# Performance work log

Measured on AMD Instinct MI355X. Metric: run time of the kernel, lower is better.

## Reference

```python
import jax, jax.numpy as jnp
import numpy as np
import math

HEADS = 8
DIM_HEAD = 64
DIM = HEADS * DIM_HEAD  # 512; to_v is Identity so dim must equal heads*dim_head
SCALE = DIM_HEAD ** -0.5


def get_slopes(n):
    def pow2(n):
        start = 2 ** (-2 ** (-(math.log2(n) - 3)))
        return [start * start ** i for i in range(n)]
    if math.log2(n).is_integer():
        return pow2(n)
    c = 2 ** math.floor(math.log2(n))
    return pow2(c) + get_slopes(2 * c)[0::2][: n - c]

SLOPES = jnp.asarray(np.array(get_slopes(HEADS), dtype=np.float32))


def setup_inputs() -> dict:
    key = jax.random.key(0)
    k1, k2, k3, k4 = jax.random.split(key, 4)
    b, n = 4, 2048
    x = jax.random.normal(k1, (b, n, DIM), dtype=jnp.float32)
    # positions: e.g. observation timestamps (days); uniform floats scaled to [0, 365)
    positions = jax.random.uniform(k2, (b, n), dtype=jnp.float32) * 365.0
    Wq = jax.random.normal(k3, (DIM, DIM), dtype=jnp.float32) * (DIM ** -0.5)
    Wk = jax.random.normal(k4, (DIM, DIM), dtype=jnp.float32) * (DIM ** -0.5)
    return {"x": x, "positions": positions, "Wq": Wq, "Wk": Wk}


def reference(x, positions, Wq, Wk):
    b, n, _ = x.shape
    # q, k projections (no bias); v = x (Identity)
    q = (x @ Wq.T).reshape(b, n, HEADS, DIM_HEAD).transpose(0, 2, 1, 3)  # b h n d
    k = (x @ Wk.T).reshape(b, n, HEADS, DIM_HEAD).transpose(0, 2, 1, 3)
    v = x.reshape(b, n, HEADS, DIM_HEAD).transpose(0, 2, 1, 3)
    dots = jnp.einsum('bhid,bhjd->bhij', q, k) * SCALE  # b h n n
    # relative_positions[b,i,j] = -|positions[b,j] - positions[b,i]|
    rel = -jnp.abs(positions[:, None, :] - positions[:, :, None])  # b n n
    alibi = SLOPES[None, :, None, None] * rel[:, None, :, :]  # b h n n
    attn = jax.nn.softmax(dots + alibi, axis=-1)
    out = jnp.einsum('bhij,bhjd->bhid', attn, v)  # b h n d
    return out.transpose(0, 2, 1, 3).reshape(b, n, DIM)
```

## Files before the change

### kernel.cpp

```cpp
#include <hip/hip_runtime.h>
#include <hip/hip_bf16.h>

typedef __bf16 bf16x8 __attribute__((ext_vector_type(8)));
typedef float f32x4 __attribute__((ext_vector_type(4)));
typedef float f32x16 __attribute__((ext_vector_type(16)));

__device__ inline unsigned short f2bf(float f) {
    __hip_bfloat16 h = __float2bfloat16(f);
    return __builtin_bit_cast(unsigned short, h);
}
__device__ inline unsigned pk2bf(float a, float b) {
    return (unsigned)f2bf(a) | ((unsigned)f2bf(b) << 16);
}
__device__ inline float exp2_fast(float x) {
    float r;
    asm("v_exp_f32 %0, %1" : "=v"(r) : "v"(x));
    return r;
}

#define QSCALE 0.1803368801111244f

__global__ __launch_bounds__(256) void xpose_v(const float* __restrict__ x,
                                               unsigned short* __restrict__ Vt) {
    const int tid = threadIdx.x;
    const int lane = tid & 63, w = tid >> 6;
    const int b = blockIdx.z, h = blockIdx.y;
    const int n = blockIdx.x * 256 + w * 64 + lane;
    const int np = (n & ~15) | (n & 3) | ((n & 4) << 1) | ((n & 8) >> 1);
    const size_t xrow = ((size_t)b * 2048 + n) * 512 + h * 64;
    const size_t vbase = ((size_t)(b * 8 + h) * 64) * 2048 + np;
#pragma unroll
    for (int d0 = 0; d0 < 64; d0 += 4) {
        float4 v = *reinterpret_cast<const float4*>(&x[xrow + d0]);
        Vt[vbase + (size_t)(d0 + 0) * 2048] = f2bf(v.x);
        Vt[vbase + (size_t)(d0 + 1) * 2048] = f2bf(v.y);
        Vt[vbase + (size_t)(d0 + 2) * 2048] = f2bf(v.z);
        Vt[vbase + (size_t)(d0 + 3) * 2048] = f2bf(v.w);
    }
}

__global__ __launch_bounds__(256) void gemm_qk(const float* __restrict__ x,
                                               const float* __restrict__ Wq,
                                               const float* __restrict__ Wk,
                                               unsigned short* __restrict__ Qb,
                                               unsigned short* __restrict__ Kb) {
    __shared__ __align__(16) unsigned short sA[128 * 40];
    __shared__ __align__(16) unsigned short sB[128 * 40];
    const int tid  = threadIdx.x;
    const int lane = tid & 63;
    const int wave = tid >> 6;
    const int wr = wave >> 1, wc = wave & 1;
    const int bm = blockIdx.x * 128;
    const int by = blockIdx.y;
    const float* __restrict__ Bsrc = (by < 4) ? Wq : Wk;
    unsigned short* __restrict__ C = (by < 4) ? Qb : Kb;
    const int bn = (by & 3) * 128;
    const float scale = (by < 4) ? QSCALE : 1.0f;
    const int tr = tid >> 1, th = (tid & 1) * 16;
    const int rl = lane & 15;
    const int kq = (lane >> 4) * 8;

    f32x4 acc[4][4];
#pragma unroll
    for (int m = 0; m < 4; ++m)
#pragma unroll
        for (int n = 0; n < 4; ++n) acc[m][n] = (f32x4){0.f, 0.f, 0.f, 0.f};

    for (int k0 = 0; k0 < 512; k0 += 32) {
        const float* ap = &x[(size_t)(bm + tr) * 512 + k0 + th];
        const float* bp = &Bsrc[(size_t)(bn + tr) * 512 + k0 + th];
        float4 a0 = *reinterpret_cast<const float4*>(ap);
        float4 a1 = *reinterpret_cast<const float4*>(ap + 4);
        float4 a2 = *reinterpret_cast<const float4*>(ap + 8);
        float4 a3 = *reinterpret_cast<const float4*>(ap + 12);
        float4 b0 = *reinterpret_cast<const float4*>(bp);
        float4 b1 = *reinterpret_cast<const float4*>(bp + 4);
        float4 b2 = *reinterpret_cast<const float4*>(bp + 8);
        float4 b3 = *reinterpret_cast<const float4*>(bp + 12);
        uint4 pa0 = {pk2bf(a0.x, a0.y), pk2bf(a0.z, a0.w), pk2bf(a1.x, a1.y), pk2bf(a1.z, a1.w)};
        uint4 pa1 = {pk2bf(a2.x, a2.y), pk2bf(a2.z, a2.w), pk2bf(a3.x, a3.y), pk2bf(a3.z, a3.w)};
        uint4 pb0 = {pk2bf(b0.x, b0.y), pk2bf(b0.z, b0.w), pk2bf(b1.x, b1.y), pk2bf(b1.z, b1.w)};
        uint4 pb1 = {pk2bf(b2.x, b2.y), pk2bf(b2.z, b2.w), pk2bf(b3.x, b3.y), pk2bf(b3.z, b3.w)};
        __syncthreads();
        *reinterpret_cast<uint4*>(&sA[tr * 40 + th])     = pa0;
        *reinterpret_cast<uint4*>(&sA[tr * 40 + th + 8]) = pa1;
        *reinterpret_cast<uint4*>(&sB[tr * 40 + th])     = pb0;
        *reinterpret_cast<uint4*>(&sB[tr * 40 + th + 8]) = pb1;
        __syncthreads();

        bf16x8 af[4], bfv[4];
#pragma unroll
        for (int m = 0; m < 4; ++m)
            af[m] = __builtin_bit_cast(bf16x8,
                *reinterpret_cast<const uint4*>(&sA[(wr * 64 + m * 16 + rl) * 40 + kq]));
#pragma unroll
        for (int n = 0; n < 4; ++n)
            bfv[n] = __builtin_bit_cast(bf16x8,
                *reinterpret_cast<const uint4*>(&sB[(wc * 64 + n * 16 + rl) * 40 + kq]));
#pragma unroll
        for (int m = 0; m < 4; ++m)
#pragma unroll
            for (int n = 0; n < 4; ++n)
                acc[m][n] = __builtin_amdgcn_mfma_f32_16x16x32_bf16(af[m], bfv[n], acc[m][n], 0, 0, 0);
    }

    const int rq = (lane >> 4) * 4;
#pragma unroll
    for (int m = 0; m < 4; ++m) {
        int r = bm + wr * 64 + m * 16 + rq;
#pragma unroll
        for (int n = 0; n < 4; ++n) {
            int c = bn + wc * 64 + n * 16 + rl;
#pragma unroll
            for (int reg = 0; reg < 4; ++reg)
                C[(size_t)(r + reg) * 512 + c] = f2bf(acc[m][n][reg] * scale);
        }
    }
}

__global__ __launch_bounds__(512, 4) void attn_fwd(const unsigned short* __restrict__ Q,
                                                   const unsigned short* __restrict__ Kb,
                                                   const unsigned short* __restrict__ Vt,
                                                   const float* __restrict__ pos,
                                                   float* __restrict__ Out) {
    __shared__ __align__(16) unsigned char smem[34304];
    char* k0b = (char*)smem;
    char* v0b = (char*)smem + 8192;
    char* k1b = (char*)smem + 16384;
    char* v1b = (char*)smem + 24576;
    float* p0b = (float*)(smem + 32768);
    float* p1b = (float*)(smem + 33024);
    float* sMl = (float*)(smem + 33280);

    const int tid  = threadIdx.x;
    const int lane = tid & 63;
    const int w    = tid >> 6;
    const int l31  = lane & 31;
    const int hi   = lane >> 5;
    const int qh   = w & 3;
    const int jp   = w >> 2;
    const int flat = blockIdx.x;
    const int xcd  = flat & 7;
    const int idx  = flat >> 3;
    const int bh   = xcd * 4 + (idx >> 4);
    const int qt   = idx & 15;
    const int b = bh >> 3, h = bh & 7;
    const int q0 = qt * 128 + qh * 32;
    const size_t rowbase = (size_t)b * 2048;
    const int hc = h * 64;
    const float slopeL = ldexpf(1.4426950408889634f, -(h + 1));

    bf16x8 qf0, qf1, qf2, qf3;
    {
        const unsigned short* qp = &Q[(rowbase + q0 + l31) * 512 + hc + hi * 8];
        qf0 = __builtin_bit_cast(bf16x8, *reinterpret_cast<const uint4*>(qp));
        qf1 = __builtin_bit_cast(bf16x8, *reinterpret_cast<const uint4*>(qp + 16));
        qf2 = __builtin_bit_cast(bf16x8, *reinterpret_cast<const uint4*>(qp + 32));
        qf3 = __builtin_bit_cast(bf16x8, *reinterpret_cast<const uint4*>(qp + 48));
    }
    const float ui = slopeL * pos[rowbase + q0 + l31];
    const bf16x8 ones = __builtin_bit_cast(bf16x8,
        (uint4){0x3F803F80u, 0x3F803F80u, 0x3F803F80u, 0x3F803F80u});

    f32x16 o0, o1, lacc;
#pragma unroll
    for (int r = 0; r < 16; ++r) { o0[r] = 0.f; o1[r] = 0.f; lacc[r] = 0.f; }

    const int sr  = tid >> 3;
    const int sce = (tid & 7) * 8;
    const int wbyte = sr * 128 + (((tid & 7) * 16) ^ ((sr & 7) << 4));
    const int kswz = (l31 & 7) << 4;

    uint4 ck, cv;
    float cpj = 0.f;

    auto stage = [&](int j0v) {
        ck = *reinterpret_cast<const uint4*>(&Kb[(rowbase + j0v + sr) * 512 + hc + sce]);
        cv = *reinterpret_cast<const uint4*>(&Vt[((size_t)bh * 64 + sr) * 2048 + j0v + sce]);
        if (tid < 64) cpj = pos[rowbase + j0v + tid];
    };
    auto writeb = [&](char* KB, char* VB, float* PB) {
        *reinterpret_cast<uint4*>(KB + wbyte) = ck;
        *reinterpret_cast<uint4*>(VB + wbyte) = cv;
        if (tid < 64) PB[tid] = slopeL * cpj;
    };
    auto compute = [&](const char* KB, const char* VB, const float* PB) {
        const char* kr = KB + (32 * jp + l31) * 128;
        f32x16 s;
#pragma unroll
        for (int r = 0; r < 16; ++r) s[r] = 0.f;
        __builtin_amdgcn_s_setprio(1);
#pragma unroll
        for (int ks = 0; ks < 4; ++ks) {
            bf16x8 kf = __builtin_bit_cast(bf16x8,
                *reinterpret_cast<const uint4*>(kr + ((ks * 32 + hi * 16) ^ kswz)));
            bf16x8 qq = (ks == 0) ? qf0 : (ks == 1) ? qf1 : (ks == 2) ? qf2 : qf3;
            s = __builtin_amdgcn_mfma_f32_32x32x16_bf16(kf, qq, s, 0, 0, 0);
        }
        __builtin_amdgcn_s_setprio(0);

#pragma unroll
        for (int t = 0; t < 4; ++t) {
            f32x4 u = *reinterpret_cast<const f32x4*>(&PB[32 * jp + 8 * t + 4 * hi]);
#pragma unroll
            for (int r = 0; r < 4; ++r)
                s[4 * t + r] = exp2_fast(s[4 * t + r] - fabsf(u[r] - ui));
        }

        bf16x8 pf0 = __builtin_bit_cast(bf16x8, (uint4){
            pk2bf(s[0], s[1]),  pk2bf(s[2], s[3]),   pk2bf(s[4], s[5]),   pk2bf(s[6], s[7])});
        bf16x8 pf1 = __builtin_bit_cast(bf16x8, (uint4){
            pk2bf(s[8], s[9]),  pk2bf(s[10], s[11]), pk2bf(s[12], s[13]), pk2bf(s[14], s[15])});

        const char* vr0 = VB + l31 * 128;
        const char* vr1 = VB + (32 + l31) * 128;
        __builtin_amdgcn_s_setprio(1);
#pragma unroll
        for (int ks = 0; ks < 2; ++ks) {
            const int cb = (64 * jp + ks * 32 + hi * 16) ^ kswz;
            bf16x8 v0 = __builtin_bit_cast(bf16x8, *reinterpret_cast<const uint4*>(vr0 + cb));
            bf16x8 v1 = __builtin_bit_cast(bf16x8, *reinterpret_cast<const uint4*>(vr1 + cb));
            bf16x8 pf = ks ? pf1 : pf0;
            o0 = __builtin_amdgcn_mfma_f32_32x32x16_bf16(v0, pf, o0, 0, 0, 0);
            o1 = __builtin_amdgcn_mfma_f32_32x32x16_bf16(v1, pf, o1, 0, 0, 0);
            lacc = __builtin_amdgcn_mfma_f32_32x32x16_bf16(ones, pf, lacc, 0, 0, 0);
        }
        __builtin_amdgcn_s_setprio(0);
    };

    stage(0);
    writeb(k0b, v0b, p0b);
    stage(64);
    __syncthreads();

    for (int t = 0; t < 32; t += 2) {
        writeb(k1b, v1b, p1b);
        if (t + 2 < 32) stage((t + 2) * 64);
        compute(k0b, v0b, p0b);
        __syncthreads();
        if (t + 2 < 32) {
            writeb(k0b, v0b, p0b);
            if (t + 3 < 32) stage((t + 3) * 64);
        }
        compute(k1b, v1b, p1b);
        __syncthreads();
    }

    const float lt = lacc[0];
    float* sM = (float*)smem;
    const int key = (lane & 7) << 2;
    if (jp == 1) {
        float* dst = sM + qh * 2048 + lane * 32;
#pragma unroll
        for (int i = 0; i < 4; ++i) {
            f32x4 t0 = {o0[4 * i], o0[4 * i + 1], o0[4 * i + 2], o0[4 * i + 3]};
            f32x4 t1 = {o1[4 * i], o1[4 * i + 1], o1[4 * i + 2], o1[4 * i + 3]};
            *reinterpret_cast<f32x4*>(dst + ((4 * i) ^ key))      = t0;
            *reinterpret_cast<f32x4*>(dst + ((16 + 4 * i) ^ key)) = t1;
        }
        sMl[qh * 64 + lane] = lt;
    }
    __syncthreads();
    if (jp == 0) {
        const float* src = sM + qh * 2048 + lane * 32;
#pragma unroll
        for (int i = 0; i < 4; ++i) {
            f32x4 t0 = *reinterpret_cast<const f32x4*>(src + ((4 * i) ^ key));
            f32x4 t1 = *reinterpret_cast<const f32x4*>(src + ((16 + 4 * i) ^ key));
#pragma unroll
            for (int r = 0; r < 4; ++r) { o0[4 * i + r] += t0[r]; o1[4 * i + r] += t1[r]; }
        }
        const float linv = 1.0f / (lt + sMl[qh * 64 + lane]);
        float* orow = &Out[(rowbase + q0 + l31) * 512 + hc];
#pragma unroll
        for (int t = 0; t < 4; ++t) {
            f32x4 a, c;
#pragma unroll
            for (int r = 0; r < 4; ++r) {
                a[r] = o0[4 * t + r] * linv;
                c[r] = o1[4 * t + r] * linv;
            }
            *reinterpret_cast<f32x4*>(orow + 8 * t + 4 * hi)      = a;
            *reinterpret_cast<f32x4*>(orow + 32 + 8 * t + 4 * hi) = c;
        }
    }
}

extern "C" void kernel_launch(void* const* d_in, const int* in_sizes, int n_in,
                              void* d_out, int out_size, void* d_ws, size_t ws_size,
                              hipStream_t stream) {
    const float* x   = (const float*)d_in[0];
    const float* pos = (const float*)d_in[1];
    const float* Wq  = (const float*)d_in[2];
    const float* Wk  = (const float*)d_in[3];
    float* out = (float*)d_out;

    unsigned short* Qb  = (unsigned short*)d_ws;
    unsigned short* Kbf = Qb  + 4194304;
    unsigned short* Vtb = Kbf + 4194304;

    xpose_v<<<dim3(8, 8, 4), dim3(256), 0, stream>>>(x, Vtb);
    gemm_qk<<<dim3(64, 8), dim3(256), 0, stream>>>(x, Wq, Wk, Qb, Kbf);
    attn_fwd<<<dim3(512), dim3(512), 0, stream>>>(Qb, Kbf, Vtb, pos, out);
}
```

Before: 92.90 us.

## Fold V transpose into QK GEMM launch; preload scaled positions; sum row totals in VALU

Removes the separate V-transpose kernel by adding extra blockIdx.y slices to the QK projection launch, which saves one kernel launch and lets the transpose overlap the GEMM. In attention, all scaled key positions for the batch row are loaded into shared memory once up front instead of being staged each tile. The softmax denominator is now accumulated as a scalar sum of exponentials plus a cross-lane shuffle, replacing the extra MFMA against a ones matrix. The trade-off is more LDS per block (42KB), which may reduce occupancy, and a different rounding path for the denominator: the sum uses fp32 p rather than bf16-rounded p.

```diff
diff --git a/kernel.cpp b/kernel.cpp
--- a/kernel.cpp
+++ b/kernel.cpp
@@ -20,38 +20,41 @@
 
 #define QSCALE 0.1803368801111244f
 
-__global__ __launch_bounds__(256) void xpose_v(const float* __restrict__ x,
-                                               unsigned short* __restrict__ Vt) {
-    const int tid = threadIdx.x;
-    const int lane = tid & 63, w = tid >> 6;
-    const int b = blockIdx.z, h = blockIdx.y;
-    const int n = blockIdx.x * 256 + w * 64 + lane;
-    const int np = (n & ~15) | (n & 3) | ((n & 4) << 1) | ((n & 8) >> 1);
-    const size_t xrow = ((size_t)b * 2048 + n) * 512 + h * 64;
-    const size_t vbase = ((size_t)(b * 8 + h) * 64) * 2048 + np;
-#pragma unroll
-    for (int d0 = 0; d0 < 64; d0 += 4) {
-        float4 v = *reinterpret_cast<const float4*>(&x[xrow + d0]);
-        Vt[vbase + (size_t)(d0 + 0) * 2048] = f2bf(v.x);
-        Vt[vbase + (size_t)(d0 + 1) * 2048] = f2bf(v.y);
-        Vt[vbase + (size_t)(d0 + 2) * 2048] = f2bf(v.z);
-        Vt[vbase + (size_t)(d0 + 3) * 2048] = f2bf(v.w);
-    }
-}
-
 __global__ __launch_bounds__(256) void gemm_qk(const float* __restrict__ x,
                                                const float* __restrict__ Wq,
                                                const float* __restrict__ Wk,
                                                unsigned short* __restrict__ Qb,
-                                               unsigned short* __restrict__ Kb) {
+                                               unsigned short* __restrict__ Kb,
+                                               unsigned short* __restrict__ Vt) {
     __shared__ __align__(16) unsigned short sA[128 * 40];
     __shared__ __align__(16) unsigned short sB[128 * 40];
     const int tid  = threadIdx.x;
+    const int by = blockIdx.y;
+
+    if (by >= 8) {
+        const int q = by - 8;
+        const int nl = tid & 127, hh = tid >> 7;
+        const int h = q * 2 + hh;
+        const int g = blockIdx.x * 128 + nl;
+        const int b = g >> 11, n = g & 2047;
+        const int np = (n & ~15) | (n & 3) | ((n & 4) << 1) | ((n & 8) >> 1);
+        const size_t xrow = ((size_t)b * 2048 + n) * 512 + h * 64;
+        const size_t vbase = ((size_t)(b * 8 + h) * 64) * 2048 + np;
+#pragma unroll
+        for (int d0 = 0; d0 < 64; d0 += 4) {
+            float4 v = *reinterpret_cast<const float4*>(&x[xrow + d0]);
+            Vt[vbase + (size_t)(d0 + 0) * 2048] = f2bf(v.x);
+            Vt[vbase + (size_t)(d0 + 1) * 2048] = f2bf(v.y);
+            Vt[vbase + (size_t)(d0 + 2) * 2048] = f2bf(v.z);
+            Vt[vbase + (size_t)(d0 + 3) * 2048] = f2bf(v.w);
+        }
+        return;
+    }
+
     const int lane = tid & 63;
     const int wave = tid >> 6;
     const int wr = wave >> 1, wc = wave & 1;
     const int bm = blockIdx.x * 128;
-    const int by = blockIdx.y;
     const float* __restrict__ Bsrc = (by < 4) ? Wq : Wk;
     unsigned short* __restrict__ C = (by < 4) ? Qb : Kb;
     const int bn = (by & 3) * 128;
@@ -123,14 +126,13 @@
                                                    const unsigned short* __restrict__ Vt,
                                                    const float* __restrict__ pos,
                                                    float* __restrict__ Out) {
-    __shared__ __align__(16) unsigned char smem[34304];
+    __shared__ __align__(16) unsigned char smem[42240];
     char* k0b = (char*)smem;
     char* v0b = (char*)smem + 8192;
     char* k1b = (char*)smem + 16384;
     char* v1b = (char*)smem + 24576;
-    float* p0b = (float*)(smem + 32768);
-    float* p1b = (float*)(smem + 33024);
-    float* sMl = (float*)(smem + 33280);
+    float* sPosT = (float*)(smem + 32768);
+    float* sMl   = (float*)(smem + 40960);
 
     const int tid  = threadIdx.x;
     const int lane = tid & 63;
@@ -159,12 +161,17 @@
         qf3 = __builtin_bit_cast(bf16x8, *reinterpret_cast<const uint4*>(qp + 48));
     }
     const float ui = slopeL * pos[rowbase + q0 + l31];
-    const bf16x8 ones = __builtin_bit_cast(bf16x8,
-        (uint4){0x3F803F80u, 0x3F803F80u, 0x3F803F80u, 0x3F803F80u});
-
-    f32x16 o0, o1, lacc;
-#pragma unroll
-    for (int r = 0; r < 16; ++r) { o0[r] = 0.f; o1[r] = 0.f; lacc[r] = 0.f; }
+
+    {
+        float4 v = reinterpret_cast<const float4*>(pos + rowbase)[tid];
+        reinterpret_cast<f32x4*>(sPosT)[tid] =
+            (f32x4){v.x * slopeL, v.y * slopeL, v.z * slopeL, v.w * slopeL};
+    }
+
+    float lloc = 0.f;
+    f32x16 o0, o1;
+#pragma unroll
+    for (int r = 0; r < 16; ++r) { o0[r] = 0.f; o1[r] = 0.f; }
 
     const int sr  = tid >> 3;
     const int sce = (tid & 7) * 8;
@@ -172,19 +179,16 @@
     const int kswz = (l31 & 7) << 4;
 
     uint4 ck, cv;
-    float cpj = 0.f;
 
     auto stage = [&](int j0v) {
         ck = *reinterpret_cast<const uint4*>(&Kb[(rowbase + j0v + sr) * 512 + hc + sce]);
         cv = *reinterpret_cast<const uint4*>(&Vt[((size_t)bh * 64 + sr) * 2048 + j0v + sce]);
-        if (tid < 64) cpj = pos[rowbase + j0v + tid];
     };
-    auto writeb = [&](char* KB, char* VB, float* PB) {
+    auto writeb = [&](char* KB, char* VB) {
         *reinterpret_cast<uint4*>(KB + wbyte) = ck;
         *reinterpret_cast<uint4*>(VB + wbyte) = cv;
-        if (tid < 64) PB[tid] = slopeL * cpj;
     };
-    auto compute = [&](const char* KB, const char* VB, const float* PB) {
+    auto compute = [&](const char* KB, const char* VB, int j0) {
         const char* kr = KB + (32 * jp + l31) * 128;
         f32x16 s;
 #pragma unroll
@@ -199,13 +203,18 @@
         }
         __builtin_amdgcn_s_setprio(0);
 
+        float ls = 0.f;
 #pragma unroll
         for (int t = 0; t < 4; ++t) {
-            f32x4 u = *reinterpret_cast<const f32x4*>(&PB[32 * jp + 8 * t + 4 * hi]);
-#pragma unroll
-            for (int r = 0; r < 4; ++r)
-                s[4 * t + r] = exp2_fast(s[4 * t + r] - fabsf(u[r] - ui));
-        }
+            f32x4 u = *reinterpret_cast<const f32x4*>(&sPosT[j0 + 32 * jp + 8 * t + 4 * hi]);
+#pragma unroll
+            for (int r = 0; r < 4; ++r) {
+                float p = exp2_fast(s[4 * t + r] - fabsf(u[r] - ui));
+                s[4 * t + r] = p;
+                ls += p;
+            }
+        }
+        lloc += ls;
 
         bf16x8 pf0 = __builtin_bit_cast(bf16x8, (uint4){
             pk2bf(s[0], s[1]),  pk2bf(s[2], s[3]),   pk2bf(s[4], s[5]),   pk2bf(s[6], s[7])});
@@ -223,30 +232,29 @@
             bf16x8 pf = ks ? pf1 : pf0;
             o0 = __builtin_amdgcn_mfma_f32_32x32x16_bf16(v0, pf, o0, 0, 0, 0);
             o1 = __builtin_amdgcn_mfma_f32_32x32x16_bf16(v1, pf, o1, 0, 0, 0);
-            lacc = __builtin_amdgcn_mfma_f32_32x32x16_bf16(ones, pf, lacc, 0, 0, 0);
         }
         __builtin_amdgcn_s_setprio(0);
     };
 
     stage(0);
-    writeb(k0b, v0b, p0b);
+    writeb(k0b, v0b);
     stage(64);
     __syncthreads();
 
     for (int t = 0; t < 32; t += 2) {
-        writeb(k1b, v1b, p1b);
+        writeb(k1b, v1b);
         if (t + 2 < 32) stage((t + 2) * 64);
-        compute(k0b, v0b, p0b);
+        compute(k0b, v0b, t * 64);
         __syncthreads();
         if (t + 2 < 32) {
-            writeb(k0b, v0b, p0b);
+            writeb(k0b, v0b);
             if (t + 3 < 32) stage((t + 3) * 64);
         }
-        compute(k1b, v1b, p1b);
+        compute(k1b, v1b, (t + 1) * 64);
         __syncthreads();
     }
 
-    const float lt = lacc[0];
+    float lt = lloc + __shfl_xor(lloc, 32, 64);
     float* sM = (float*)smem;
     const int key = (lane & 7) << 2;
     if (jp == 1) {
@@ -299,7 +307,6 @@
     unsigned short* Kbf = Qb  + 4194304;
     unsigned short* Vtb = Kbf + 4194304;
 
-    xpose_v<<<dim3(8, 8, 4), dim3(256), 0, stream>>>(x, Vtb);
-    gemm_qk<<<dim3(64, 8), dim3(256), 0, stream>>>(x, Wq, Wk, Qb, Kbf);
+    gemm_qk<<<dim3(64, 12), dim3(256), 0, stream>>>(x, Wq, Wk, Qb, Kbf, Vtb);
     attn_fwd<<<dim3(512), dim3(512), 0, stream>>>(Qb, Kbf, Vtb, pos, out);
 }
```

Result: faster. 79.70 us (-14.2%).
